# Performance work log

Hardware: AMD Instinct MI355X
Metric: run time of the kernel (lower is better)

Reference implementation:

```python
import jax, jax.numpy as jnp
import numpy as np

GAMA = 10.0


def setup_inputs() -> dict:
    key = jax.random.key(0)
    k1, k2, k3, k4, k5 = jax.random.split(key, 5)
    n_class, n_center, hidden, batch = 100, 4, 512, 512
    init_mu, sigma_lower = 0.1, 10.0
    x = jax.random.normal(k1, (batch, hidden), dtype=jnp.float32)
    y = jax.random.randint(k2, (batch,), 0, n_class, dtype=jnp.int32).astype(jnp.int64)
    mu_base_vector = jax.random.normal(k3, (hidden,), dtype=jnp.float32)
    class_mu = jax.random.uniform(k4, (n_class, n_center, hidden), dtype=jnp.float32) * (2 * init_mu) - init_mu
    class_sigma = jnp.ones((n_class, n_center, hidden), dtype=jnp.float32) * sigma_lower
    class_pi = jax.random.uniform(k5, (n_class, n_center), dtype=jnp.float32)
    class_pi = class_pi / class_pi.sum(axis=1, keepdims=True)
    return {"x": x, "y": y, "mu_base_vector": mu_base_vector,
            "class_mu": class_mu, "class_sigma": class_sigma, "class_pi": class_pi}


def reference(x, y, mu_base_vector, class_mu, class_sigma, class_pi):
    # Cluster.log_likelihood(x, y, reduction='mean')
    B, H = x.shape
    # scale() detaches mu_base_vector
    xs = (x - jax.lax.stop_gradient(mu_base_vector)) / GAMA  # [B, H]
    # log_probs: broadcasted diagonal-Gaussian log-likelihood
    diff = xs[None, None, :, :] - class_mu[:, :, None, :]            # [C, K, B, H]
    log_exp = -0.5 * jnp.sum(diff * diff * (class_sigma * class_sigma)[:, :, None, :], axis=-1)  # [C, K, B]
    log_det = jnp.sum(jnp.log(class_sigma), axis=-1)[:, :, None]     # [C, K, 1]
    const = -0.5 * H * jnp.log(2.0 * jnp.pi).astype(x.dtype)
    log_probs = jnp.transpose(log_exp + log_det + const, (2, 0, 1))  # [B, C, K]
    # one-hot class selection == gather along class axis
    lp_sel = jnp.take_along_axis(log_probs, y[:, None, None].astype(jnp.int32), axis=1)[:, 0, :]  # [B, K]
    log_pi = jnp.log(jax.nn.softmax(class_pi, axis=1))[y]            # [B, K]
    log_scores = log_pi + lp_sel                                     # [B, K]
    log_likelihood = jnp.max(log_scores, axis=1)                     # [B]
    return jnp.mean(log_likelihood)
```

## Files before the change

### kernel.cpp

```cpp
#include <hip/hip_runtime.h>
#include <math.h>

#define KC 4
#define GAMA_INV 0.1f
#define NITER 2

__global__ void __launch_bounds__(64)
row_ll_kernel(const float* __restrict__ x,
              const int* __restrict__ y,
              const float* __restrict__ mu_base,
              const float* __restrict__ class_mu,
              const float* __restrict__ class_sigma,
              const float* __restrict__ class_pi,
              float* __restrict__ rowll, int H) {
    const int i    = blockIdx.x;
    const int lane = threadIdx.x;
    const int c    = y[i];

    const float4* __restrict__ x4  = (const float4*)(x + (size_t)i * H);
    const float4* __restrict__ mb4 = (const float4*)mu_base;

    float4 xs[NITER];
    #pragma unroll
    for (int j = 0; j < NITER; ++j) {
        float4 a = x4[lane + 64 * j];
        float4 b = mb4[lane + 64 * j];
        xs[j].x = (a.x - b.x) * GAMA_INV;
        xs[j].y = (a.y - b.y) * GAMA_INV;
        xs[j].z = (a.z - b.z) * GAMA_INV;
        xs[j].w = (a.w - b.w) * GAMA_INV;
    }

    float sc[KC];
    #pragma unroll
    for (int k = 0; k < KC; ++k) {
        const float4* __restrict__ mu4 =
            (const float4*)(class_mu + ((size_t)c * KC + k) * H);
        const float4* __restrict__ sg4 =
            (const float4*)(class_sigma + ((size_t)c * KC + k) * H);
        float acc = 0.0f, ldet = 0.0f;
        #pragma unroll
        for (int j = 0; j < NITER; ++j) {
            float4 m = mu4[lane + 64 * j];
            float4 s = sg4[lane + 64 * j];
            float dx = xs[j].x - m.x, dy = xs[j].y - m.y;
            float dz = xs[j].z - m.z, dw = xs[j].w - m.w;
            acc = fmaf(dx * dx, s.x * s.x, acc);
            acc = fmaf(dy * dy, s.y * s.y, acc);
            acc = fmaf(dz * dz, s.z * s.z, acc);
            acc = fmaf(dw * dw, s.w * s.w, acc);
            ldet += __logf(s.x) + __logf(s.y) + __logf(s.z) + __logf(s.w);
        }
        #pragma unroll
        for (int off = 1; off < 64; off <<= 1) {
            acc  += __shfl_xor(acc,  off, 64);
            ldet += __shfl_xor(ldet, off, 64);
        }
        sc[k] = -0.5f * acc + ldet;
    }

    if (lane == 0) {
        float p[KC];
        float m = -INFINITY;
        #pragma unroll
        for (int k = 0; k < KC; ++k) {
            p[k] = class_pi[(size_t)c * KC + k];
            m = fmaxf(m, p[k]);
        }
        float se = 0.0f;
        #pragma unroll
        for (int k = 0; k < KC; ++k) se += __expf(p[k] - m);
        float lse = m + __logf(se);

        const float cst = -0.5f * (float)H * __logf(2.0f * (float)M_PI);
        float mx = -INFINITY;
        #pragma unroll
        for (int k = 0; k < KC; ++k)
            mx = fmaxf(mx, (p[k] - lse) + sc[k] + cst);
        rowll[i] = mx;
    }
}

__global__ void __launch_bounds__(64)
mean_kernel(const float* __restrict__ rowll, float* __restrict__ out, int B) {
    const int lane = threadIdx.x;
    float s = 0.0f;
    for (int j = lane; j < B; j += 64) s += rowll[j];
    #pragma unroll
    for (int off = 1; off < 64; off <<= 1) s += __shfl_xor(s, off, 64);
    if (lane == 0) out[0] = s / (float)B;
}

extern "C" void kernel_launch(void* const* d_in, const int* in_sizes, int n_in,
                              void* d_out, int out_size, void* d_ws, size_t ws_size,
                              hipStream_t stream) {
    const float* x        = (const float*)d_in[0];
    const int*   y        = (const int*)  d_in[1];
    const float* mu_base  = (const float*)d_in[2];
    const float* class_mu = (const float*)d_in[3];
    const float* class_sg = (const float*)d_in[4];
    const float* class_pi = (const float*)d_in[5];
    float* out   = (float*)d_out;
    float* rowll = (float*)d_ws;

    const int B = in_sizes[1];
    const int H = in_sizes[2];

    row_ll_kernel<<<B, 64, 0, stream>>>(x, y, mu_base, class_mu, class_sg,
                                        class_pi, rowll, H);
    mean_kernel<<<1, 64, 0, stream>>>(rowll, out, B);
}
```

Baseline: 69.40 us.

## Fuse row likelihood and mean into one cooperative kernel with grid sync

Merges the per-row log-likelihood kernel and the mean-reduction kernel into a single cooperative launch, using a grid-wide sync before block 0 sums the row results. All mu and sigma loads are issued up front to increase memory-level parallelism. The per-element log of sigma is replaced by a product of sigmas followed by one log2 per lane, which cuts transcendental work but risks overflow or underflow of the product and reorders the reduction. Cooperative launch and grid sync add their own overhead and require all 512 blocks to be co-resident.

```diff
diff --git a/kernel.cpp b/kernel.cpp
--- a/kernel.cpp
+++ b/kernel.cpp
@@ -1,18 +1,24 @@
 #include <hip/hip_runtime.h>
+#include <hip/hip_cooperative_groups.h>
 #include <math.h>
 
 #define KC 4
 #define GAMA_INV 0.1f
 #define NITER 2
+#define LN2F 0.69314718055994530942f
+
+namespace cg = cooperative_groups;
 
 __global__ void __launch_bounds__(64)
-row_ll_kernel(const float* __restrict__ x,
-              const int* __restrict__ y,
-              const float* __restrict__ mu_base,
-              const float* __restrict__ class_mu,
-              const float* __restrict__ class_sigma,
-              const float* __restrict__ class_pi,
-              float* __restrict__ rowll, int H) {
+fused_ll_kernel(const float* __restrict__ x,
+                const int* __restrict__ y,
+                const float* __restrict__ mu_base,
+                const float* __restrict__ class_mu,
+                const float* __restrict__ class_sigma,
+                const float* __restrict__ class_pi,
+                float* __restrict__ rowll,
+                float* __restrict__ out,
+                int H, int B) {
     const int i    = blockIdx.x;
     const int lane = threadIdx.x;
     const int c    = y[i];
@@ -31,32 +37,42 @@
         xs[j].w = (a.w - b.w) * GAMA_INV;
     }
 
-    float sc[KC];
+    float4 mu[KC][NITER], sg[KC][NITER];
     #pragma unroll
     for (int k = 0; k < KC; ++k) {
         const float4* __restrict__ mu4 =
             (const float4*)(class_mu + ((size_t)c * KC + k) * H);
         const float4* __restrict__ sg4 =
             (const float4*)(class_sigma + ((size_t)c * KC + k) * H);
-        float acc = 0.0f, ldet = 0.0f;
         #pragma unroll
         for (int j = 0; j < NITER; ++j) {
-            float4 m = mu4[lane + 64 * j];
-            float4 s = sg4[lane + 64 * j];
+            mu[k][j] = mu4[lane + 64 * j];
+            sg[k][j] = sg4[lane + 64 * j];
+        }
+    }
+
+    float sc[KC];
+    #pragma unroll
+    for (int k = 0; k < KC; ++k) {
+        float acc = 0.0f;
+        float prod = 1.0f;
+        #pragma unroll
+        for (int j = 0; j < NITER; ++j) {
+            float4 m = mu[k][j];
+            float4 s = sg[k][j];
             float dx = xs[j].x - m.x, dy = xs[j].y - m.y;
             float dz = xs[j].z - m.z, dw = xs[j].w - m.w;
             acc = fmaf(dx * dx, s.x * s.x, acc);
             acc = fmaf(dy * dy, s.y * s.y, acc);
             acc = fmaf(dz * dz, s.z * s.z, acc);
             acc = fmaf(dw * dw, s.w * s.w, acc);
-            ldet += __logf(s.x) + __logf(s.y) + __logf(s.z) + __logf(s.w);
+            prod *= (s.x * s.y) * (s.z * s.w);
         }
+        float v = fmaf(-0.5f, acc, LN2F * __log2f(prod));
         #pragma unroll
-        for (int off = 1; off < 64; off <<= 1) {
-            acc  += __shfl_xor(acc,  off, 64);
-            ldet += __shfl_xor(ldet, off, 64);
-        }
-        sc[k] = -0.5f * acc + ldet;
+        for (int off = 1; off < 64; off <<= 1)
+            v += __shfl_xor(v, off, 64);
+        sc[k] = v;
     }
 
     if (lane == 0) {
@@ -77,18 +93,21 @@
         #pragma unroll
         for (int k = 0; k < KC; ++k)
             mx = fmaxf(mx, (p[k] - lse) + sc[k] + cst);
-        rowll[i] = mx;
+        __hip_atomic_store(&rowll[i], mx, __ATOMIC_RELAXED,
+                           __HIP_MEMORY_SCOPE_AGENT);
     }
-}
 
-__global__ void __launch_bounds__(64)
-mean_kernel(const float* __restrict__ rowll, float* __restrict__ out, int B) {
-    const int lane = threadIdx.x;
-    float s = 0.0f;
-    for (int j = lane; j < B; j += 64) s += rowll[j];
-    #pragma unroll
-    for (int off = 1; off < 64; off <<= 1) s += __shfl_xor(s, off, 64);
-    if (lane == 0) out[0] = s / (float)B;
+    cg::this_grid().sync();
+
+    if (i == 0) {
+        float s = 0.0f;
+        for (int j = lane; j < B; j += 64)
+            s += __hip_atomic_load(&rowll[j], __ATOMIC_RELAXED,
+                                   __HIP_MEMORY_SCOPE_AGENT);
+        #pragma unroll
+        for (int off = 1; off < 64; off <<= 1) s += __shfl_xor(s, off, 64);
+        if (lane == 0) out[0] = s / (float)B;
+    }
 }
 
 extern "C" void kernel_launch(void* const* d_in, const int* in_sizes, int n_in,
@@ -106,7 +125,13 @@
     const int B = in_sizes[1];
     const int H = in_sizes[2];
 
-    row_ll_kernel<<<B, 64, 0, stream>>>(x, y, mu_base, class_mu, class_sg,
-                                        class_pi, rowll, H);
-    mean_kernel<<<1, 64, 0, stream>>>(rowll, out, B);
+    void* args[] = { (void*)&x, (void*)&y, (void*)&mu_base, (void*)&class_mu,
+                     (void*)&class_sg, (void*)&class_pi, (void*)&rowll,
+                     (void*)&out, (void*)&B, (void*)&H };
+    void* args_fixed[] = { (void*)&x, (void*)&y, (void*)&mu_base,
+                           (void*)&class_mu, (void*)&class_sg, (void*)&class_pi,
+                           (void*)&rowll, (void*)&out, (void*)&H, (void*)&B };
+    (void)args;
+    hipLaunchCooperativeKernel((const void*)fused_ll_kernel, dim3(B), dim3(64),
+                               args_fixed, 0, stream);
 }
```

New measurement: 133.6 us. 1.92x slower.
